# Kernel tuning notes

Hardware: AMD Instinct MI355X
Metric: run time of the kernel (lower is better)

The kernel has to match this reference:

```python
import jax, jax.numpy as jnp
import numpy as np

N_NODES = 30000
NEG_SLOPE = 0.2  # PyG GATConv default leaky_relu slope


def gat_conv(x, src, dst, W, a_src, a_dst, b, num_nodes, concat):
    """One PyG-style GATConv layer (add_self_loops already applied to src/dst).
    x: [N, F_in]; W: [F_in, H*C]; a_src, a_dst: [H, C]; b: [H*C] or [C].
    """
    H, C = a_src.shape
    h = (x @ W).reshape(num_nodes, H, C)                     # [N, H, C]
    alpha_src = jnp.einsum('nhc,hc->nh', h, a_src)           # [N, H]
    alpha_dst = jnp.einsum('nhc,hc->nh', h, a_dst)           # [N, H]
    e = jax.nn.leaky_relu(alpha_src[src] + alpha_dst[dst], NEG_SLOPE)  # [E, H]
    # scatter-softmax over incoming edges of each dst node
    e_max = jax.ops.segment_max(e, dst, num_segments=num_nodes)        # [N, H]
    e_exp = jnp.exp(e - e_max[dst])                                    # [E, H]
    denom = jax.ops.segment_sum(e_exp, dst, num_segments=num_nodes)    # [N, H]
    alpha = e_exp / denom[dst]                                         # [E, H]
    msg = h[src] * alpha[:, :, None]                                   # [E, H, C]
    out = jax.ops.segment_sum(msg, dst, num_segments=num_nodes)        # [N, H, C]
    out = out.reshape(num_nodes, H * C) if concat else out.mean(axis=1)
    return out + b


def _glorot(key, shape):
    fan = sum(shape[:2]) if len(shape) > 1 else shape[0] * 2
    return jax.random.normal(key, shape, dtype=jnp.float32) * np.sqrt(2.0 / fan)


def setup_inputs() -> dict:
    key = jax.random.key(0)
    ks = jax.random.split(key, 16)
    n, f_in, heads = N_NODES, 256, 4
    x = jax.random.normal(ks[0], (n, f_in), dtype=jnp.float32)
    edge_index = jax.random.randint(ks[1], (2, 480000), 0, n, dtype=jnp.int64)
    inp = {
        'x': x, 'edge_index': edge_index,
        'W1': _glorot(ks[2], (f_in, heads * 128)),
        'a1s': _glorot(ks[3], (heads, 128)), 'a1d': _glorot(ks[4], (heads, 128)),
        'b1': jnp.zeros((heads * 128,), jnp.float32),
        'W2': _glorot(ks[5], (heads * 128, heads * 128)),
        'a2s': _glorot(ks[6], (heads, 128)), 'a2d': _glorot(ks[7], (heads, 128)),
        'b2': jnp.zeros((heads * 128,), jnp.float32),
        'W3': _glorot(ks[8], (heads * 128, heads * 64)),
        'a3s': _glorot(ks[9], (heads, 64)), 'a3d': _glorot(ks[10], (heads, 64)),
        'b3': jnp.zeros((heads * 64,), jnp.float32),
        # conv4: 256 -> 64, 1 head, mean (concat=False)
        'W4': _glorot(ks[11], (heads * 64, 64)),
        'a4s': _glorot(ks[12], (1, 64)), 'a4d': _glorot(ks[13], (1, 64)),
        'b4': jnp.zeros((64,), jnp.float32),
    }
    return inp


def reference(x, edge_index, W1, a1s, a1d, b1, W2, a2s, a2d, b2,
              W3, a3s, a3d, b3, W4, a4s, a4d, b4):
    n = x.shape[0]
    # PyG GATConv default add_self_loops=True
    loops = jnp.arange(n, dtype=edge_index.dtype)
    src = jnp.concatenate([edge_index[0], loops])
    dst = jnp.concatenate([edge_index[1], loops])
    h = jax.nn.relu(gat_conv(x, src, dst, W1, a1s, a1d, b1, n, True))
    h = jax.nn.relu(gat_conv(h, src, dst, W2, a2s, a2d, b2, n, True))
    h = jax.nn.relu(gat_conv(h, src, dst, W3, a3s, a3d, b3, n, True))
    h = jax.nn.relu(gat_conv(h, src, dst, W4, a4s, a4d, b4, n, False))
    return h
```

## Files before the change

kernel.cpp:

```cpp
#include <hip/hip_runtime.h>
#include <hip/hip_fp16.h>
#include <math.h>


typedef __attribute__((ext_vector_type(8))) __bf16 bf16x8;
typedef __attribute__((ext_vector_type(4))) float floatx4;
typedef __attribute__((ext_vector_type(8))) unsigned short usv8;
typedef __attribute__((ext_vector_type(4))) unsigned short usv4;

#define DEG_CAP 256

__device__ __forceinline__ unsigned short f2bf(float f) {
    unsigned int u = __float_as_uint(f);
    u += 0x7fff + ((u >> 16) & 1);
    return (unsigned short)(u >> 16);
}
__device__ __forceinline__ float bf2f(unsigned short u) {
    return __uint_as_float(((unsigned int)u) << 16);
}
__device__ __forceinline__ float lrelu(float e) {
    return (e > 0.f) ? e : 0.2f * e;
}
__device__ __forceinline__ void gload16(const void* g, void* l) {
    __builtin_amdgcn_global_load_lds(
        (const __attribute__((address_space(1))) void*)g,
        (__attribute__((address_space(3))) void*)l, 16, 0, 0);
}

static __global__ void zero_float(float* __restrict__ p, int n) {
    int i = blockIdx.x * blockDim.x + threadIdx.x;
    if (i < n) p[i] = 0.f;
}
static __global__ void zero_int(int* __restrict__ p, int n) {
    int i = blockIdx.x * blockDim.x + threadIdx.x;
    if (i < n) p[i] = 0;
}

static __global__ void hist_kernel(const int* __restrict__ ei, int e0, int n_nodes,
                                   int* __restrict__ counts) {
    int e = blockIdx.x * blockDim.x + threadIdx.x;
    int et = e0 + n_nodes;
    if (e >= et) return;
    int d = (e < e0) ? ei[e0 + e] : (e - e0);
    atomicAdd(&counts[d], 1);
}

static __global__ void scan_kernel(const int* __restrict__ counts,
                                   int* __restrict__ row_ptr,
                                   int* __restrict__ cursor, int n) {
    __shared__ int sdata[1024];
    int tid = threadIdx.x;
    int per = (n + 1023) / 1024;
    int start = tid * per;
    int stop = min(start + per, n);
    if (start > n) start = n;
    int s = 0;
    for (int i = start; i < stop; i++) s += counts[i];
    sdata[tid] = s;
    __syncthreads();
    for (int off = 1; off < 1024; off <<= 1) {
        int t = (tid >= off) ? sdata[tid - off] : 0;
        __syncthreads();
        sdata[tid] += t;
        __syncthreads();
    }
    int run = sdata[tid] - s;
    for (int i = start; i < stop; i++) {
        row_ptr[i] = run;
        cursor[i] = run;
        run += counts[i];
    }
    if (stop == n) row_ptr[n] = run;
}

static __global__ void scatter_kernel(const int* __restrict__ ei, int e0, int n_nodes,
                                      int* __restrict__ cursor,
                                      int* __restrict__ src_sorted) {
    int e = blockIdx.x * blockDim.x + threadIdx.x;
    int et = e0 + n_nodes;
    if (e >= et) return;
    int s, d;
    if (e < e0) { s = ei[e]; d = ei[e0 + e]; } else { s = e - e0; d = s; }
    int pos = atomicAdd(&cursor[d], 1);
    src_sorted[pos] = s;
}

static __global__ void convA_kernel(const float* __restrict__ X,
                                    unsigned short* __restrict__ A, int M, int K) {
    int idx = blockIdx.x * 256 + threadIdx.x;
    if (idx >= M * K) return;
    int m = idx / K, k = idx % K;
    float v = X[idx];
    unsigned short hi = f2bf(v);
    size_t base = (size_t)m * (2 * K);
    A[base + k] = hi;
    A[base + K + k] = f2bf(v - bf2f(hi));
}

__device__ __forceinline__ void convW_one(const float* W, unsigned short* BT,
                                          int idx, int K, int N) {
    int n = idx / K, k = idx % K;
    float v = (n < N) ? W[(size_t)k * N + n] : 0.f;
    unsigned short hi = f2bf(v);
    size_t base = (size_t)n * (2 * K);
    BT[base + k] = hi;
    BT[base + K + k] = f2bf(v - bf2f(hi));
}

static __global__ void convW_all(const float* __restrict__ W1, unsigned short* __restrict__ BT1,
                                 const float* __restrict__ W2, unsigned short* __restrict__ BT2,
                                 const float* __restrict__ W3, unsigned short* __restrict__ BT3,
                                 const float* __restrict__ W4, unsigned short* __restrict__ BT4) {
    int idx = blockIdx.x * 256 + threadIdx.x;
    if (idx < 131072) { convW_one(W1, BT1, idx, 256, 512); return; }
    idx -= 131072;
    if (idx < 262144) { convW_one(W2, BT2, idx, 512, 512); return; }
    idx -= 262144;
    if (idx < 131072) { convW_one(W3, BT3, idx, 512, 256); return; }
    idx -= 131072;
    if (idx < 32768)  { convW_one(W4, BT4, idx, 256, 64); }
}

#define BM 128
#define BN 128
#define BKK 64

__launch_bounds__(256, 2)
static __global__ void gemm_mfma(const unsigned short* __restrict__ A,
                                 const unsigned short* __restrict__ B,
                                 __half* __restrict__ C, int M, int K, int N,
                                 int xcols, int mblocks,
                                 const float* __restrict__ asv,
                                 const float* __restrict__ adv,
                                 float* __restrict__ as_out,
                                 float* __restrict__ ad_out,
                                 int Hh, int Cc) {
    __shared__ __align__(16) unsigned short lds[4 * BM * BKK];
    const int tid  = threadIdx.x;
    const int lane = tid & 63;
    const int wave = tid >> 6;

    const int id = blockIdx.x;
    const int band = id / (8 * xcols);
    const int rem = id - band * 8 * xcols;
    const int band_rows = min(8, mblocks - band * 8);
    const int ry = rem % band_rows;
    const int rx = rem / band_rows;
    const int r0 = (band * 8 + ry) * BM;
    const int c0 = rx * BN;

    const int wm = (wave >> 1) * 64;
    const int wn = (wave & 1) * 64;
    const int q   = lane >> 4;
    const int m16 = lane & 15;

    floatx4 acc[4][4];
#pragma unroll
    for (int i = 0; i < 4; i++)
#pragma unroll
        for (int j = 0; j < 4; j++) acc[i][j] = {0.f, 0.f, 0.f, 0.f};

    const size_t sA = (size_t)(2 * K);
    const size_t sB = (size_t)(2 * K);
    char* ldsb = (char*)lds;

#pragma unroll 1
    for (int k0 = 0; k0 < K; k0 += BKK) {
        __syncthreads();
#pragma unroll
        for (int c = 0; c < 4; c++) {
            int slot = c * 256 + tid;
            int row = slot >> 3;
            int gc  = (slot & 7) ^ (row & 7);
            const unsigned short* Ab = A + (size_t)(r0 + row) * sA + k0 + gc * 8;
            const unsigned short* Bb = B + (size_t)(c0 + row) * sB + k0 + gc * 8;
            gload16(Ab,     ldsb + slot * 16);
            gload16(Ab + K, ldsb + 16384 + slot * 16);
            gload16(Bb,     ldsb + 32768 + slot * 16);
            gload16(Bb + K, ldsb + 49152 + slot * 16);
        }
        __syncthreads();
#pragma unroll
        for (int ks = 0; ks < 2; ks++) {
            bf16x8 ah[4], al[4], bh[4], bl[4];
#pragma unroll
            for (int i = 0; i < 4; i++) {
                int row = wm + i * 16 + m16;
                int ch  = (q + ks * 4) ^ (row & 7);
                int off = (row * 8 + ch) * 16;
                ah[i] = *(const bf16x8*)(ldsb + off);
                al[i] = *(const bf16x8*)(ldsb + 16384 + off);
            }
#pragma unroll
            for (int j = 0; j < 4; j++) {
                int row = wn + j * 16 + m16;
                int ch  = (q + ks * 4) ^ (row & 7);
                int off = (row * 8 + ch) * 16;
                bh[j] = *(const bf16x8*)(ldsb + 32768 + off);
                bl[j] = *(const bf16x8*)(ldsb + 49152 + off);
            }
#pragma unroll
            for (int i = 0; i < 4; i++)
#pragma unroll
                for (int j = 0; j < 4; j++) {
                    acc[i][j] = __builtin_amdgcn_mfma_f32_16x16x32_bf16(
                        ah[i], bh[j], acc[i][j], 0, 0, 0);
                    acc[i][j] = __builtin_amdgcn_mfma_f32_16x16x32_bf16(
                        al[i], bh[j], acc[i][j], 0, 0, 0);
                    acc[i][j] = __builtin_amdgcn_mfma_f32_16x16x32_bf16(
                        ah[i], bl[j], acc[i][j], 0, 0, 0);
                }
        }
    }
#pragma unroll
    for (int i = 0; i < 4; i++)
#pragma unroll
        for (int j = 0; j < 4; j++)
#pragma unroll
            for (int r = 0; r < 4; r++) {
                int row = r0 + wm + i * 16 + q * 4 + r;
                int col = c0 + wn + j * 16 + m16;
                if (row < M && col < N)
                    C[(size_t)row * N + col] = __float2half(acc[i][j][r]);
            }
    if (c0 + wn < N) {
        int head = (c0 + wn) / Cc;
#pragma unroll
        for (int i = 0; i < 4; i++)
#pragma unroll
            for (int r = 0; r < 4; r++) {
                float ps = 0.f, pd = 0.f;
#pragma unroll
                for (int j = 0; j < 4; j++) {
                    int c = c0 + wn + j * 16 + m16;
                    float v = acc[i][j][r];
                    ps = fmaf(v, asv[c], ps);
                    pd = fmaf(v, adv[c], pd);
                }
#pragma unroll
                for (int off = 1; off < 16; off <<= 1) {
                    ps += __shfl_xor(ps, off);
                    pd += __shfl_xor(pd, off);
                }
                if (m16 == 0) {
                    int row = r0 + wm + i * 16 + q * 4 + r;
                    if (row < M) {
                        atomicAdd(&as_out[(size_t)row * Hh + head], ps);
                        atomicAdd(&ad_out[(size_t)row * Hh + head], pd);
                    }
                }
            }
    }
}

template <int R>
__device__ __forceinline__ void accum_row(const __half* hptr, size_t off, float w,
                                          float* acc) {
    const __half* p = hptr + off;
    if constexpr (R == 8) {
        float4 raw = *(const float4*)p;
        const __half* hv = (const __half*)&raw;
#pragma unroll
        for (int r = 0; r < 8; r++) acc[r] = fmaf(__half2float(hv[r]), w, acc[r]);
    } else if constexpr (R == 4) {
        float2 raw = *(const float2*)p;
        const __half* hv = (const __half*)&raw;
#pragma unroll
        for (int r = 0; r < 4; r++) acc[r] = fmaf(__half2float(hv[r]), w, acc[r]);
    } else {
        acc[0] = fmaf(__half2float(*p), w, acc[0]);
    }
}

template <int H, int C, bool BF16OUT>
__launch_bounds__(256)
static __global__ void agg_kernel(const __half* __restrict__ h,
                                  const float* __restrict__ as_arr,
                                  const float* __restrict__ ad_arr,
                                  const int* __restrict__ row_ptr,
                                  const int* __restrict__ src_sorted,
                                  const float* __restrict__ bias,
                                  float* __restrict__ outf,
                                  unsigned short* __restrict__ outb,
                                  float* __restrict__ znext_as,
                                  float* __restrict__ znext_ad, int n_nodes) {
    constexpr int R = H * C / 64;
    constexpr int G = 64 / H;
    constexpr int K = H * C;
    __shared__ float lds_e[4][DEG_CAP * H];
    int wave = threadIdx.x >> 6;
    int lane = threadIdx.x & 63;
    int n = blockIdx.x * 4 + wave;
    if (n >= n_nodes) return;
    int beg = row_ptr[n], end = row_ptr[n + 1];
    float* we = lds_e[wave];

    float ad_h[H], m_h[H], l_h[H];
#pragma unroll
    for (int hh = 0; hh < H; hh++) {
        ad_h[hh] = ad_arr[(size_t)n * H + hh];
        m_h[hh] = -INFINITY;
        l_h[hh] = 0.f;
    }
    for (int base = beg; base < end; base += 64) {
        int j = base + lane;
        bool ok = j < end;
        float e_h[H];
        if (ok) {
            int s = src_sorted[j];
            if constexpr (H == 4) {
                float4 a = ((const float4*)as_arr)[s];
                e_h[0] = lrelu(a.x + ad_h[0]);
                e_h[1] = lrelu(a.y + ad_h[1]);
                e_h[2] = lrelu(a.z + ad_h[2]);
                e_h[3] = lrelu(a.w + ad_h[3]);
            } else {
                e_h[0] = lrelu(as_arr[s] + ad_h[0]);
            }
            int idx = j - beg;
            if (idx < DEG_CAP) {
                if constexpr (H == 4) {
                    *(float4*)&we[idx * 4] = make_float4(e_h[0], e_h[1], e_h[2], e_h[3]);
                } else {
                    we[idx] = e_h[0];
                }
            }
        } else {
#pragma unroll
            for (int hh = 0; hh < H; hh++) e_h[hh] = -INFINITY;
        }
#pragma unroll
        for (int hh = 0; hh < H; hh++) {
            float cm = e_h[hh];
#pragma unroll
            for (int off = 1; off < 64; off <<= 1) cm = fmaxf(cm, __shfl_xor(cm, off));
            float newm = fmaxf(m_h[hh], cm);
            float p = ok ? __expf(e_h[hh] - newm) : 0.f;
#pragma unroll
            for (int off = 1; off < 64; off <<= 1) p += __shfl_xor(p, off);
            l_h[hh] = l_h[hh] * __expf(m_h[hh] - newm) + p;
            m_h[hh] = newm;
        }
    }
    int myh = lane / G;
    float mm, adm, inv;
    if constexpr (H == 4) {
        mm  = m_h[0];  mm  = (myh == 1) ? m_h[1] : mm;  mm  = (myh == 2) ? m_h[2] : mm;  mm  = (myh == 3) ? m_h[3] : mm;
        float ll = l_h[0]; ll = (myh == 1) ? l_h[1] : ll; ll = (myh == 2) ? l_h[2] : ll; ll = (myh == 3) ? l_h[3] : ll;
        adm = ad_h[0]; adm = (myh == 1) ? ad_h[1] : adm; adm = (myh == 2) ? ad_h[2] : adm; adm = (myh == 3) ? ad_h[3] : adm;
        inv = 1.f / ll;
    } else {
        mm = m_h[0]; adm = ad_h[0]; inv = 1.f / l_h[0];
    }

    float acc[R];
#pragma unroll
    for (int r = 0; r < R; r++) acc[r] = 0.f;

    int j = beg;
    for (; j + 3 < end; j += 4) {
        int i0 = j - beg;
        int s0 = src_sorted[j];
        int s1 = src_sorted[j + 1];
        int s2 = src_sorted[j + 2];
        int s3 = src_sorted[j + 3];
        float e0, e1, e2, e3;
        if (i0 + 3 < DEG_CAP) {
            e0 = we[(i0 + 0) * H + myh];
            e1 = we[(i0 + 1) * H + myh];
            e2 = we[(i0 + 2) * H + myh];
            e3 = we[(i0 + 3) * H + myh];
        } else {
            e0 = lrelu(as_arr[(size_t)s0 * H + myh] + adm);
            e1 = lrelu(as_arr[(size_t)s1 * H + myh] + adm);
            e2 = lrelu(as_arr[(size_t)s2 * H + myh] + adm);
            e3 = lrelu(as_arr[(size_t)s3 * H + myh] + adm);
        }
        float w0 = __expf(e0 - mm) * inv;
        float w1 = __expf(e1 - mm) * inv;
        float w2 = __expf(e2 - mm) * inv;
        float w3 = __expf(e3 - mm) * inv;
        accum_row<R>(h, (size_t)s0 * K + lane * R, w0, acc);
        accum_row<R>(h, (size_t)s1 * K + lane * R, w1, acc);
        accum_row<R>(h, (size_t)s2 * K + lane * R, w2, acc);
        accum_row<R>(h, (size_t)s3 * K + lane * R, w3, acc);
    }
    for (; j < end; j++) {
        int i0 = j - beg;
        int s0 = src_sorted[j];
        float e0 = (i0 < DEG_CAP) ? we[i0 * H + myh]
                                  : lrelu(as_arr[(size_t)s0 * H + myh] + adm);
        float w0 = __expf(e0 - mm) * inv;
        accum_row<R>(h, (size_t)s0 * K + lane * R, w0, acc);
    }

    if (znext_as != nullptr && lane == 0) {
        if constexpr (H == 4) {
            *(float4*)&znext_as[(size_t)n * 4] = make_float4(0.f, 0.f, 0.f, 0.f);
            *(float4*)&znext_ad[(size_t)n * 4] = make_float4(0.f, 0.f, 0.f, 0.f);
        } else {
            znext_as[n] = 0.f;
            znext_ad[n] = 0.f;
        }
    }
    float vout[R];
#pragma unroll
    for (int r = 0; r < R; r++)
        vout[r] = fmaxf(acc[r] + bias[lane * R + r], 0.f);

    if constexpr (BF16OUT) {
        unsigned short hi[R], lo[R];
#pragma unroll
        for (int r = 0; r < R; r++) {
            hi[r] = f2bf(vout[r]);
            lo[r] = f2bf(vout[r] - bf2f(hi[r]));
        }
        size_t base = (size_t)n * (2 * K) + lane * R;
        if constexpr (R == 8) {
            usv8 vh = {hi[0], hi[1], hi[2], hi[3], hi[4], hi[5], hi[6], hi[7]};
            usv8 vl = {lo[0], lo[1], lo[2], lo[3], lo[4], lo[5], lo[6], lo[7]};
            *(usv8*)(outb + base) = vh;
            *(usv8*)(outb + base + K) = vl;
        } else if constexpr (R == 4) {
            usv4 vh = {hi[0], hi[1], hi[2], hi[3]};
            usv4 vl = {lo[0], lo[1], lo[2], lo[3]};
            *(usv4*)(outb + base) = vh;
            *(usv4*)(outb + base + K) = vl;
        } else {
#pragma unroll
            for (int r = 0; r < R; r++) {
                outb[base + r] = hi[r];
                outb[base + K + r] = lo[r];
            }
        }
    } else {
#pragma unroll
        for (int r = 0; r < R; r++)
            outf[(size_t)n * K + lane * R + r] = vout[r];
    }
}


static inline size_t align_up(size_t x) { return (x + 255) & ~(size_t)255; }

extern "C" void kernel_launch(void* const* d_in, const int* in_sizes, int n_in,
                              void* d_out, int out_size, void* d_ws, size_t ws_size,
                              hipStream_t stream) {
    const float* x   = (const float*)d_in[0];
    const int*   ei  = (const int*)d_in[1];
    const float* W1  = (const float*)d_in[2];
    const float* a1s = (const float*)d_in[3];
    const float* a1d = (const float*)d_in[4];
    const float* b1  = (const float*)d_in[5];
    const float* W2  = (const float*)d_in[6];
    const float* a2s = (const float*)d_in[7];
    const float* a2d = (const float*)d_in[8];
    const float* b2  = (const float*)d_in[9];
    const float* W3  = (const float*)d_in[10];
    const float* a3s = (const float*)d_in[11];
    const float* a3d = (const float*)d_in[12];
    const float* b3  = (const float*)d_in[13];
    const float* W4  = (const float*)d_in[14];
    const float* a4s = (const float*)d_in[15];
    const float* a4d = (const float*)d_in[16];
    const float* b4  = (const float*)d_in[17];

    const int n  = in_sizes[0] / 256;
    const int e0 = in_sizes[1] / 2;
    const int et = e0 + n;
    const int Mpad = ((n + 127) / 128) * 128;

    char* w = (char*)d_ws;
    unsigned short* slotA = (unsigned short*)w;  w += align_up((size_t)Mpad * 1024 * 2);
    __half* hbuf = (__half*)w;                   w += align_up((size_t)n * 512 * 4);
    unsigned short* WT1 = (unsigned short*)w;    w += align_up((size_t)512 * 512 * 2);
    unsigned short* WT2 = (unsigned short*)w;    w += align_up((size_t)512 * 1024 * 2);
    unsigned short* WT3 = (unsigned short*)w;    w += align_up((size_t)256 * 1024 * 2);
    unsigned short* WT4 = (unsigned short*)w;    w += align_up((size_t)128 * 512 * 2);
    float* asA = (float*)w;                      w += align_up((size_t)n * 4 * 4);
    float* adA = (float*)w;                      w += align_up((size_t)n * 4 * 4);
    float* asB = (float*)w;                      w += align_up((size_t)n * 4 * 4);
    float* adB = (float*)w;                      w += align_up((size_t)n * 4 * 4);
    int* row_ptr = (int*)w;                      w += align_up((size_t)(n + 1) * 4);
    int* counts  = (int*)w;                      w += align_up((size_t)n * 4);
    int* cursor  = (int*)w;                      w += align_up((size_t)n * 4);
    int* src_sorted = (int*)w;                   w += align_up((size_t)et * 4);
    (void)ws_size;

    dim3 blk(256);
    int nodeblocks = (n + 3) / 4;

    zero_int<<<(n + 255) / 256, 256, 0, stream>>>(counts, n);
    hist_kernel<<<(et + 255) / 256, 256, 0, stream>>>(ei, e0, n, counts);
    scan_kernel<<<1, 1024, 0, stream>>>(counts, row_ptr, cursor, n);
    scatter_kernel<<<(et + 255) / 256, 256, 0, stream>>>(ei, e0, n, cursor, src_sorted);

    convA_kernel<<<((n * 256) + 255) / 256, blk, 0, stream>>>(x, slotA, n, 256);
    convW_all<<<(557056 + 255) / 256, blk, 0, stream>>>(W1, WT1, W2, WT2, W3, WT3, W4, WT4);
    zero_float<<<(n * 8 + 255) / 256, blk, 0, stream>>>(asA, n * 8);

    const int mblocks = Mpad / 128;

    gemm_mfma<<<dim3(4 * mblocks), blk, 0, stream>>>(slotA, WT1, hbuf, n, 256, 512, 4, mblocks,
                                                     a1s, a1d, asA, adA, 4, 128);
    agg_kernel<4, 128, true><<<nodeblocks, blk, 0, stream>>>(hbuf, asA, adA, row_ptr, src_sorted, b1, nullptr, slotA, asB, adB, n);

    gemm_mfma<<<dim3(4 * mblocks), blk, 0, stream>>>(slotA, WT2, hbuf, n, 512, 512, 4, mblocks,
                                                     a2s, a2d, asB, adB, 4, 128);
    agg_kernel<4, 128, true><<<nodeblocks, blk, 0, stream>>>(hbuf, asB, adB, row_ptr, src_sorted, b2, nullptr, slotA, asA, adA, n);

    gemm_mfma<<<dim3(2 * mblocks), blk, 0, stream>>>(slotA, WT3, hbuf, n, 512, 256, 2, mblocks,
                                                     a3s, a3d, asA, adA, 4, 64);
    agg_kernel<4, 64, true><<<nodeblocks, blk, 0, stream>>>(hbuf, asA, adA, row_ptr, src_sorted, b3, nullptr, slotA, asB, adB, n);

    gemm_mfma<<<dim3(1 * mblocks), blk, 0, stream>>>(slotA, WT4, hbuf, n, 256, 64, 1, mblocks,
                                                     a4s, a4d, asB, adB, 1, 64);
    agg_kernel<1, 64, false><<<nodeblocks, blk, 0, stream>>>(hbuf, asB, adB, row_ptr, src_sorted, b4, (float*)d_out, nullptr, nullptr, nullptr, n);
}
```

Baseline: 630.9 us.

## Halve GEMM K-tile for higher occupancy, cache edge sources in LDS, unroll aggregation by eight

The GEMM K-step drops from 64 to 32, which halves LDS use per block. The swizzle is reworked for the narrower 4-chunk rows, and launch bounds are raised to three blocks per CU to increase occupancy. The aggregation kernel now stores each edge's source index in LDS during the softmax pass, so the gather pass reads it from LDS instead of global memory. The gather loop is also unrolled by 8 to keep more row loads in flight. The risks are more barriers per K, register pressure under the tighter launch bound, and extra LDS per aggregation block.

Result: slower. 646.0 us (+2.4%).

```diff
diff --git a/kernel.cpp b/kernel.cpp
--- a/kernel.cpp
+++ b/kernel.cpp
@@ -123,9 +123,9 @@
 
 #define BM 128
 #define BN 128
-#define BKK 64
-
-__launch_bounds__(256, 2)
+#define BKK 32
+
+__launch_bounds__(256, 3)
 static __global__ void gemm_mfma(const unsigned short* __restrict__ A,
                                  const unsigned short* __restrict__ B,
                                  __half* __restrict__ C, int M, int K, int N,
@@ -168,49 +168,46 @@
     for (int k0 = 0; k0 < K; k0 += BKK) {
         __syncthreads();
 #pragma unroll
-        for (int c = 0; c < 4; c++) {
+        for (int c = 0; c < 2; c++) {
             int slot = c * 256 + tid;
-            int row = slot >> 3;
-            int gc  = (slot & 7) ^ (row & 7);
+            int row = slot >> 2;
+            int gc  = (slot & 3) ^ ((row >> 1) & 3);
             const unsigned short* Ab = A + (size_t)(r0 + row) * sA + k0 + gc * 8;
             const unsigned short* Bb = B + (size_t)(c0 + row) * sB + k0 + gc * 8;
             gload16(Ab,     ldsb + slot * 16);
-            gload16(Ab + K, ldsb + 16384 + slot * 16);
-            gload16(Bb,     ldsb + 32768 + slot * 16);
-            gload16(Bb + K, ldsb + 49152 + slot * 16);
+            gload16(Ab + K, ldsb + 8192 + slot * 16);
+            gload16(Bb,     ldsb + 16384 + slot * 16);
+            gload16(Bb + K, ldsb + 24576 + slot * 16);
         }
         __syncthreads();
-#pragma unroll
-        for (int ks = 0; ks < 2; ks++) {
-            bf16x8 ah[4], al[4], bh[4], bl[4];
-#pragma unroll
-            for (int i = 0; i < 4; i++) {
-                int row = wm + i * 16 + m16;
-                int ch  = (q + ks * 4) ^ (row & 7);
-                int off = (row * 8 + ch) * 16;
-                ah[i] = *(const bf16x8*)(ldsb + off);
-                al[i] = *(const bf16x8*)(ldsb + 16384 + off);
-            }
+        bf16x8 ah[4], al[4], bh[4], bl[4];
+#pragma unroll
+        for (int i = 0; i < 4; i++) {
+            int row = wm + i * 16 + m16;
+            int ch  = q ^ ((row >> 1) & 3);
+            int off = (row * 4 + ch) * 16;
+            ah[i] = *(const bf16x8*)(ldsb + off);
+            al[i] = *(const bf16x8*)(ldsb + 8192 + off);
+        }
+#pragma unroll
+        for (int j = 0; j < 4; j++) {
+            int row = wn + j * 16 + m16;
+            int ch  = q ^ ((row >> 1) & 3);
+            int off = (row * 4 + ch) * 16;
+            bh[j] = *(const bf16x8*)(ldsb + 16384 + off);
+            bl[j] = *(const bf16x8*)(ldsb + 24576 + off);
+        }
+#pragma unroll
+        for (int i = 0; i < 4; i++)
 #pragma unroll
             for (int j = 0; j < 4; j++) {
-                int row = wn + j * 16 + m16;
-                int ch  = (q + ks * 4) ^ (row & 7);
-                int off = (row * 8 + ch) * 16;
-                bh[j] = *(const bf16x8*)(ldsb + 32768 + off);
-                bl[j] = *(const bf16x8*)(ldsb + 49152 + off);
-            }
-#pragma unroll
-            for (int i = 0; i < 4; i++)
-#pragma unroll
-                for (int j = 0; j < 4; j++) {
-                    acc[i][j] = __builtin_amdgcn_mfma_f32_16x16x32_bf16(
-                        ah[i], bh[j], acc[i][j], 0, 0, 0);
-                    acc[i][j] = __builtin_amdgcn_mfma_f32_16x16x32_bf16(
-                        al[i], bh[j], acc[i][j], 0, 0, 0);
-                    acc[i][j] = __builtin_amdgcn_mfma_f32_16x16x32_bf16(
-                        ah[i], bl[j], acc[i][j], 0, 0, 0);
-                }
-        }
+                acc[i][j] = __builtin_amdgcn_mfma_f32_16x16x32_bf16(
+                    ah[i], bh[j], acc[i][j], 0, 0, 0);
+                acc[i][j] = __builtin_amdgcn_mfma_f32_16x16x32_bf16(
+                    al[i], bh[j], acc[i][j], 0, 0, 0);
+                acc[i][j] = __builtin_amdgcn_mfma_f32_16x16x32_bf16(
+                    ah[i], bl[j], acc[i][j], 0, 0, 0);
+            }
     }
 #pragma unroll
     for (int i = 0; i < 4; i++)
@@ -288,12 +285,14 @@
     constexpr int G = 64 / H;
     constexpr int K = H * C;
     __shared__ float lds_e[4][DEG_CAP * H];
+    __shared__ int   lds_s[4][DEG_CAP];
     int wave = threadIdx.x >> 6;
     int lane = threadIdx.x & 63;
     int n = blockIdx.x * 4 + wave;
     if (n >= n_nodes) return;
     int beg = row_ptr[n], end = row_ptr[n + 1];
     float* we = lds_e[wave];
+    int*   ls = lds_s[wave];
 
     float ad_h[H], m_h[H], l_h[H];
 #pragma unroll
@@ -319,6 +318,7 @@
             }
             int idx = j - beg;
             if (idx < DEG_CAP) {
+                ls[idx] = s;
                 if constexpr (H == 4) {
                     *(float4*)&we[idx * 4] = make_float4(e_h[0], e_h[1], e_h[2], e_h[3]);
                 } else {
@@ -358,38 +358,41 @@
     for (int r = 0; r < R; r++) acc[r] = 0.f;
 
     int j = beg;
-    for (; j + 3 < end; j += 4) {
+    for (; j + 7 < end; j += 8) {
         int i0 = j - beg;
-        int s0 = src_sorted[j];
-        int s1 = src_sorted[j + 1];
-        int s2 = src_sorted[j + 2];
-        int s3 = src_sorted[j + 3];
-        float e0, e1, e2, e3;
-        if (i0 + 3 < DEG_CAP) {
-            e0 = we[(i0 + 0) * H + myh];
-            e1 = we[(i0 + 1) * H + myh];
-            e2 = we[(i0 + 2) * H + myh];
-            e3 = we[(i0 + 3) * H + myh];
+        int ss[8];
+        float ee[8];
+        if (i0 + 7 < DEG_CAP) {
+#pragma unroll
+            for (int u = 0; u < 8; u++) {
+                ss[u] = ls[i0 + u];
+                ee[u] = we[(i0 + u) * H + myh];
+            }
         } else {
-            e0 = lrelu(as_arr[(size_t)s0 * H + myh] + adm);
-            e1 = lrelu(as_arr[(size_t)s1 * H + myh] + adm);
-            e2 = lrelu(as_arr[(size_t)s2 * H + myh] + adm);
-            e3 = lrelu(as_arr[(size_t)s3 * H + myh] + adm);
-        }
-        float w0 = __expf(e0 - mm) * inv;
-        float w1 = __expf(e1 - mm) * inv;
-        float w2 = __expf(e2 - mm) * inv;
-        float w3 = __expf(e3 - mm) * inv;
-        accum_row<R>(h, (size_t)s0 * K + lane * R, w0, acc);
-        accum_row<R>(h, (size_t)s1 * K + lane * R, w1, acc);
-        accum_row<R>(h, (size_t)s2 * K + lane * R, w2, acc);
-        accum_row<R>(h, (size_t)s3 * K + lane * R, w3, acc);
+#pragma unroll
+            for (int u = 0; u < 8; u++) {
+                ss[u] = src_sorted[j + u];
+                ee[u] = lrelu(as_arr[(size_t)ss[u] * H + myh] + adm);
+            }
+        }
+        float ww[8];
+#pragma unroll
+        for (int u = 0; u < 8; u++) ww[u] = __expf(ee[u] - mm) * inv;
+#pragma unroll
+        for (int u = 0; u < 8; u++)
+            accum_row<R>(h, (size_t)ss[u] * K + lane * R, ww[u], acc);
     }
     for (; j < end; j++) {
         int i0 = j - beg;
-        int s0 = src_sorted[j];
-        float e0 = (i0 < DEG_CAP) ? we[i0 * H + myh]
-                                  : lrelu(as_arr[(size_t)s0 * H + myh] + adm);
+        int s0;
+        float e0;
+        if (i0 < DEG_CAP) {
+            s0 = ls[i0];
+            e0 = we[i0 * H + myh];
+        } else {
+            s0 = src_sorted[j];
+            e0 = lrelu(as_arr[(size_t)s0 * H + myh] + adm);
+        }
         float w0 = __expf(e0 - mm) * inv;
         accum_row<R>(h, (size_t)s0 * K + lane * R, w0, acc);
     }
```
